# Kernel optimization log

Measured on AMD Instinct MI355X. Metric: run time of the kernel, lower is better.

The kernel has to match this reference:

```python
import jax, jax.numpy as jnp
import numpy as np

EPS = 1e-12

def _layernorm(x, gamma, beta):
    m = jnp.mean(x, axis=-1, keepdims=True)
    v = jnp.mean((x - m) ** 2, axis=-1, keepdims=True)
    return (x - m) * jax.lax.rsqrt(v + EPS) * gamma + beta

def _gcn(x, node_emb, time_emb, W_pool, b_pool, gamma, beta):
    # x: [B, N, C]; node_emb: [N, D]; time_emb: [D]
    e = _layernorm(node_emb + time_emb[None, :], gamma, beta)          # [N, D] (dropout off: eval mode)
    A = jax.nn.softmax(e @ e.T, axis=1)                                 # [N, N] dynamic adjacency
    weights = jnp.einsum('nd,dkio->nkio', e, W_pool)                    # [N, 2, C, O] node-adaptive weights
    bias = e @ b_pool                                                   # [N, O]
    # supports = [I, A]; I support is identity -> x itself
    x_g = jnp.stack([x, jnp.einsum('nm,bmc->bnc', A, x)], axis=2)       # [B, N, 2, C]
    return jnp.einsum('bnki,nkio->bno', x_g, weights) + bias            # [B, N, O]

def setup_inputs() -> dict:
    key = jax.random.key(0)
    ks = jax.random.split(key, 16)
    B, N, Din, H, D = 64, 2048, 2, 64, 16
    C = Din + H
    inp = {
        'x': jax.random.normal(ks[0], (B, N, Din), jnp.float32),
        'state': jax.random.normal(ks[1], (B, N, H), jnp.float32),
        'node_embeddings': jax.random.normal(ks[2], (N, D), jnp.float32),
        'time_embeddings': jax.random.normal(ks[3], (D,), jnp.float32),
    }
    for i, g in enumerate(['z', 'r', 'u']):
        inp[f'W_{g}'] = jax.random.normal(ks[4 + 2 * i], (D, 2, C, H), jnp.float32) * 0.02
        inp[f'b_{g}'] = jax.random.normal(ks[5 + 2 * i], (D, H), jnp.float32) * 0.02
        inp[f'gamma_{g}'] = jnp.ones((D,), jnp.float32)
        inp[f'beta_{g}'] = jnp.zeros((D,), jnp.float32)
    return inp

def reference(x, state, node_embeddings, time_embeddings,
              W_z, b_z, gamma_z, beta_z,
              W_r, b_r, gamma_r, beta_r,
              W_u, b_u, gamma_u, beta_u):
    xs = jnp.concatenate([x, state], axis=-1)                           # [B, N, Din+H]
    z = jax.nn.sigmoid(_gcn(xs, node_embeddings, time_embeddings, W_z, b_z, gamma_z, beta_z))
    r = jax.nn.sigmoid(_gcn(xs, node_embeddings, time_embeddings, W_r, b_r, gamma_r, beta_r))
    cand = jnp.concatenate([x, z * state], axis=-1)
    hc = jnp.tanh(_gcn(cand, node_embeddings, time_embeddings, W_u, b_u, gamma_u, beta_u))
    return r * state + (1.0 - r) * hc
```

## Files before the change

kernel.cpp:

```cpp
#include <hip/hip_runtime.h>
#include <hip/hip_bf16.h>
#include <math.h>


typedef __attribute__((ext_vector_type(4))) float f4;
typedef __attribute__((ext_vector_type(8))) short s8;

#define B_   64
#define N_   2048
#define DIN  2
#define H_   64
#define D_   16
#define C_   66
#define KI   132
#define KIP  160
#define CB   4224

#define GLD16(gp, lp) __builtin_amdgcn_global_load_lds((const __attribute__((address_space(1))) void*)(gp), (__attribute__((address_space(3))) void*)(lp), 16, 0, 0)

static __device__ __forceinline__ ushort f2bf(float v) {
  __hip_bfloat16 h = __float2bfloat16(v);
  return *(ushort*)&h;
}
static __device__ __forceinline__ float bf2f(ushort u) {
  __hip_bfloat16 h = *(__hip_bfloat16*)&u;
  return __bfloat162float(h);
}
static __device__ __forceinline__ uint packbf(float a, float b) {
  return ((uint)f2bf(b) << 16) | f2bf(a);
}

__global__ void k_e(const float* __restrict__ node, const float* __restrict__ timee,
                    const float* __restrict__ g0, const float* __restrict__ b0,
                    const float* __restrict__ g1, const float* __restrict__ b1,
                    const float* __restrict__ g2, const float* __restrict__ b2,
                    float* __restrict__ e, ushort* __restrict__ ebf) {
  int n = blockIdx.x * blockDim.x + threadIdx.x;
  if (n >= N_) return;
  float v[D_]; float m = 0.f;
  #pragma unroll
  for (int d = 0; d < D_; ++d) { v[d] = node[n * D_ + d] + timee[d]; m += v[d]; }
  m *= (1.0f / D_);
  float var = 0.f;
  #pragma unroll
  for (int d = 0; d < D_; ++d) { float t = v[d] - m; var += t * t; }
  var *= (1.0f / D_);
  float r = rsqrtf(var + 1e-12f);
  float y[D_];
  #pragma unroll
  for (int d = 0; d < D_; ++d) y[d] = (v[d] - m) * r;
  const float* gs[3] = {g0, g1, g2};
  const float* bs[3] = {b0, b1, b2};
  #pragma unroll
  for (int g = 0; g < 3; ++g) {
    #pragma unroll
    for (int d = 0; d < D_; d += 2) {
      float o0 = y[d] * gs[g][d] + bs[g][d];
      float o1 = y[d + 1] * gs[g][d + 1] + bs[g][d + 1];
      e[g * N_ * D_ + n * D_ + d] = o0;
      e[g * N_ * D_ + n * D_ + d + 1] = o1;
      *(uint*)&ebf[g * N_ * D_ + n * D_ + d] = packbf(o0, o1);
    }
  }
}

__global__ __launch_bounds__(256)
void k_attn(const ushort* __restrict__ ebf, __hip_bfloat16* __restrict__ A) {
  __shared__ __align__(16) ushort eb[N_ * D_];
  __shared__ float red[4][16];
  const int t = threadIdx.x;
  const ushort* eg = ebf + (size_t)blockIdx.z * (N_ * D_);
  {
    const uint4* src = (const uint4*)eg;
    uint4* dst = (uint4*)eb;
    #pragma unroll
    for (int i = 0; i < 16; ++i) dst[i * 256 + t] = src[i * 256 + t];
  }
  __syncthreads();
  const int lane = t & 63, w = t >> 6;
  const int l15 = lane & 15, q = lane >> 4;
  const int r0 = blockIdx.x * 16;
  s8 rf = {0, 0, 0, 0, 0, 0, 0, 0};
  if (q < 2) rf = *(const s8*)&eb[(r0 + l15) * D_ + q * 8];
  const int c0 = w * 512;
  f4 acc[32];
  #pragma unroll
  for (int tl = 0; tl < 32; ++tl) {
    s8 cf = {0, 0, 0, 0, 0, 0, 0, 0};
    if (q < 2) cf = *(const s8*)&eb[(c0 + tl * 16 + l15) * D_ + q * 8];
    acc[tl] = __builtin_amdgcn_mfma_f32_16x16x32_bf16(cf, rf, (f4)0.0f, 0, 0, 0);
  }
  float m = acc[0][0];
  #pragma unroll
  for (int tl = 0; tl < 32; ++tl) {
    #pragma unroll
    for (int rg = 0; rg < 4; ++rg) m = fmaxf(m, acc[tl][rg]);
  }
  m = fmaxf(m, __shfl_xor(m, 16, 64));
  m = fmaxf(m, __shfl_xor(m, 32, 64));
  if (lane < 16) red[w][l15] = m;
  __syncthreads();
  const float gm = fmaxf(fmaxf(red[0][l15], red[1][l15]), fmaxf(red[2][l15], red[3][l15]));
  __syncthreads();
  float ps = 0.f;
  #pragma unroll
  for (int tl = 0; tl < 32; ++tl) {
    #pragma unroll
    for (int rg = 0; rg < 4; ++rg) {
      float v = __expf(acc[tl][rg] - gm);
      acc[tl][rg] = v;
      ps += v;
    }
  }
  ps += __shfl_xor(ps, 16, 64);
  ps += __shfl_xor(ps, 32, 64);
  if (lane < 16) red[w][l15] = ps;
  __syncthreads();
  const float inv = 1.0f / (red[0][l15] + red[1][l15] + red[2][l15] + red[3][l15]);
  ushort* Ar = (ushort*)A + (size_t)blockIdx.z * ((size_t)N_ * N_) +
               (size_t)(r0 + l15) * N_ + c0 + q * 4;
  #pragma unroll
  for (int tl = 0; tl < 32; ++tl) {
    uint2 pk;
    pk.x = packbf(acc[tl][0] * inv, acc[tl][1] * inv);
    pk.y = packbf(acc[tl][2] * inv, acc[tl][3] * inv);
    *(uint2*)&Ar[tl * 16] = pk;
  }
}

template <int MODE>
__global__ __launch_bounds__(256)
void k_buildX(const float* __restrict__ x, const float* __restrict__ state,
              const __hip_bfloat16* __restrict__ zbuf, __hip_bfloat16* __restrict__ XT) {
  constexpr int LDM = 72;
  __shared__ __align__(16) ushort T[C_ * LDM];
  const int t = threadIdx.x;
  const int m0 = blockIdx.x * 64, b = blockIdx.y;
  const int m = t >> 2, hq = t & 3;
  {
    const float* sp = state + ((size_t)b * N_ + m0 + m) * H_ + hq * 16;
    float sv[16];
    #pragma unroll
    for (int i = 0; i < 16; i += 4) {
      float4 v = *(const float4*)(sp + i);
      sv[i] = v.x; sv[i + 1] = v.y; sv[i + 2] = v.z; sv[i + 3] = v.w;
    }
    if (MODE) {
      const ushort* zp = (const ushort*)zbuf + ((size_t)b * N_ + m0 + m) * H_ + hq * 16;
      uint4 z0 = *(const uint4*)&zp[0], z1 = *(const uint4*)&zp[8];
      uint zw[8] = {z0.x, z0.y, z0.z, z0.w, z1.x, z1.y, z1.z, z1.w};
      #pragma unroll
      for (int i = 0; i < 8; ++i) {
        sv[2 * i]     *= bf2f((ushort)(zw[i] & 0xffffu));
        sv[2 * i + 1] *= bf2f((ushort)(zw[i] >> 16));
      }
    }
    #pragma unroll
    for (int i = 0; i < 16; ++i) T[(DIN + hq * 16 + i) * LDM + m] = f2bf(sv[i]);
    if (t < 64) {
      const float2 xv = *(const float2*)&x[((size_t)b * N_ + m0 + t) * DIN];
      T[0 * LDM + t] = f2bf(xv.x);
      T[1 * LDM + t] = f2bf(xv.y);
    }
  }
  __syncthreads();
  {
    int r = t >> 2, ch = t & 3;
    ushort* dst = (ushort*)XT + (size_t)(b * C_ + r) * N_ + m0 + ch * 16;
    *(uint4*)&dst[0] = *(uint4*)&T[r * LDM + ch * 16];
    *(uint4*)&dst[8] = *(uint4*)&T[r * LDM + ch * 16 + 8];
    if (t < 8) {
      r = 64 + (t >> 2);
      ushort* dst2 = (ushort*)XT + (size_t)(b * C_ + r) * N_ + m0 + ch * 16;
      *(uint4*)&dst2[0] = *(uint4*)&T[r * LDM + ch * 16];
      *(uint4*)&dst2[8] = *(uint4*)&T[r * LDM + ch * 16 + 8];
    }
  }
}

__global__ __launch_bounds__(256)
void k_gemm(const __hip_bfloat16* __restrict__ Abase, size_t astride,
            const __hip_bfloat16* __restrict__ XT,
            __hip_bfloat16* __restrict__ Ybase, size_t ystride) {
  __shared__ __align__(16) ushort At[2][128 * 32];
  __shared__ __align__(16) ushort Xt[2][128 * 32];
  const int t = threadIdx.x;
  const int nwg = gridDim.x * gridDim.y * gridDim.z;
  const int orig = blockIdx.x + gridDim.x * (blockIdx.y + gridDim.y * blockIdx.z);
  const int chunk = nwg >> 3;
  const int swz = (orig & 7) * chunk + (orig >> 3);
  const int bx = swz % gridDim.x;
  const int rest = swz / gridDim.x;
  const int by = rest % gridDim.y;
  const int bz = rest / gridDim.y;
  const int j0 = bx * 128, r0 = by * 128;
  const ushort* Ag = (const ushort*)Abase + (size_t)bz * astride;
  ushort* Y = (ushort*)Ybase + (size_t)bz * ystride;
  const int lane = t & 63, w = t >> 6;
  const int rowa = w * 32 + (lane >> 2);
  const int kc = (((lane & 3) ^ ((lane >> 3) & 3)) * 8);
  const ushort* pA0 = Ag + (size_t)(r0 + rowa) * N_ + kc;
  const ushort* pA1 = pA0 + 16 * N_;
  const ushort* pX0 = (const ushort*)XT + (size_t)(j0 + rowa) * N_ + kc;
  const ushort* pX1 = pX0 + 16 * N_;
  const int l15 = t & 15, q = (t >> 4) & 3;
  const int qs = (q ^ ((l15 >> 1) & 3)) * 8;
  const int wr = (w >> 1) * 64, wc = (w & 1) * 64;
  f4 acc[4][4];
  #pragma unroll
  for (int i = 0; i < 4; ++i)
    #pragma unroll
    for (int jj = 0; jj < 4; ++jj) acc[i][jj] = (f4)0.0f;
  GLD16(pA0, &At[0][(w * 32) * 32]);
  GLD16(pA1, &At[0][(w * 32 + 16) * 32]);
  GLD16(pX0, &Xt[0][(w * 32) * 32]);
  GLD16(pX1, &Xt[0][(w * 32 + 16) * 32]);
  pA0 += 32; pA1 += 32; pX0 += 32; pX1 += 32;
  int cur = 0;
  for (int k0 = 0; k0 < N_; k0 += 32) {
    if (k0 + 32 < N_) {
      const int nx = cur ^ 1;
      GLD16(pA0, &At[nx][(w * 32) * 32]);
      GLD16(pA1, &At[nx][(w * 32 + 16) * 32]);
      GLD16(pX0, &Xt[nx][(w * 32) * 32]);
      GLD16(pX1, &Xt[nx][(w * 32 + 16) * 32]);
      pA0 += 32; pA1 += 32; pX0 += 32; pX1 += 32;
      asm volatile("s_waitcnt vmcnt(4)" ::: "memory");
    } else {
      asm volatile("s_waitcnt vmcnt(0)" ::: "memory");
    }
    __builtin_amdgcn_s_barrier();
    __builtin_amdgcn_sched_barrier(0);
    s8 af[4], bfr[4];
    #pragma unroll
    for (int mi = 0; mi < 4; ++mi)
      af[mi] = *(const s8*)&At[cur][(wr + mi * 16 + l15) * 32 + qs];
    #pragma unroll
    for (int ni = 0; ni < 4; ++ni)
      bfr[ni] = *(const s8*)&Xt[cur][(wc + ni * 16 + l15) * 32 + qs];
    __builtin_amdgcn_s_setprio(1);
    #pragma unroll
    for (int mi = 0; mi < 4; ++mi)
      #pragma unroll
      for (int ni = 0; ni < 4; ++ni)
        acc[mi][ni] = __builtin_amdgcn_mfma_f32_16x16x32_bf16(af[mi], bfr[ni], acc[mi][ni], 0, 0, 0);
    __builtin_amdgcn_s_setprio(0);
    __builtin_amdgcn_s_barrier();
    cur ^= 1;
  }
  #pragma unroll
  for (int mi = 0; mi < 4; ++mi) {
    int rr = r0 + wr + mi * 16 + q * 4;
    #pragma unroll
    for (int ni = 0; ni < 4; ++ni) {
      int cc = j0 + wc + ni * 16 + l15;
      #pragma unroll
      for (int rg = 0; rg < 4; ++rg)
        Y[(size_t)(rr + rg) * CB + cc] = f2bf(acc[mi][ni][rg]);
    }
  }
}

__global__ __launch_bounds__(256)
void k_wmat(const float* __restrict__ eg, const float* __restrict__ Wp, ushort* __restrict__ Wm) {
  constexpr int TRS = 36;
  __shared__ float Wl[16 * 8 * 64];
  __shared__ ushort Tr[8 * 64 * TRS];
  const int t = threadIdx.x;
  const int n0 = blockIdx.x * 8;
  const int y = blockIdx.y;
  const int o = t & 63, w = t >> 6;
  const int ng = w & 1, krh = (w >> 1) * 4;
  float er[4][16];
  #pragma unroll
  for (int j = 0; j < 4; ++j) {
    const float* ep = eg + (size_t)(n0 + ng * 4 + j) * D_;
    #pragma unroll
    for (int d = 0; d < D_; d += 4) {
      float4 v = *(const float4*)(ep + d);
      er[j][d] = v.x; er[j][d + 1] = v.y; er[j][d + 2] = v.z; er[j][d + 3] = v.w;
    }
  }
  const int ngroups = (y == 3) ? 2 : 1;
  for (int g = 0; g < ngroups; ++g) {
    const int kic0 = y * 4 + g * 4;
    for (int kk = 0; kk < 4; ++kk) {
      const int kic = kic0 + kk;
      __syncthreads();
      #pragma unroll
      for (int it = 0; it < 8; ++it) {
        int f = it * 256 + t;
        int d = f >> 7, rem = f & 127, kr = rem >> 4, o4 = rem & 15;
        int ki = kic * 8 + kr;
        float4 v;
        if (ki < KI) v = *(const float4*)&Wp[((size_t)d * KI + ki) * 64 + o4 * 4];
        else { v.x = 0.f; v.y = 0.f; v.z = 0.f; v.w = 0.f; }
        *(float4*)&Wl[f * 4] = v;
      }
      __syncthreads();
      float a[4][4];
      #pragma unroll
      for (int j = 0; j < 4; ++j)
        #pragma unroll
        for (int k = 0; k < 4; ++k) a[j][k] = 0.f;
      for (int d = 0; d < D_; ++d) {
        float w4[4];
        #pragma unroll
        for (int k = 0; k < 4; ++k) w4[k] = Wl[(d * 8 + krh + k) * 64 + o];
        #pragma unroll
        for (int j = 0; j < 4; ++j)
          #pragma unroll
          for (int k = 0; k < 4; ++k) a[j][k] = fmaf(er[j][d], w4[k], a[j][k]);
      }
      #pragma unroll
      for (int j = 0; j < 4; ++j) {
        ushort* tr = &Tr[((ng * 4 + j) * 64 + o) * TRS + kk * 8 + krh];
        *(uint*)&tr[0] = packbf(a[j][0], a[j][1]);
        *(uint*)&tr[2] = packbf(a[j][2], a[j][3]);
      }
    }
    __syncthreads();
    const int k0 = kic0 * 8;
    #pragma unroll
    for (int p = 0; p < 8; ++p) {
      int u = p * 256 + t;
      int nl = u >> 8, oo = (u >> 2) & 63, qq = u & 3;
      const ushort* tr = &Tr[(nl * 64 + oo) * TRS + qq * 8];
      uint2 lo = *(const uint2*)&tr[0];
      uint2 hi = *(const uint2*)&tr[4];
      uint4 vv; vv.x = lo.x; vv.y = lo.y; vv.z = hi.x; vv.w = hi.y;
      *(uint4*)&Wm[((size_t)(n0 + nl) * 64 + oo) * KIP + k0 + qq * 8] = vv;
    }
  }
}

template <int MODE>
__global__ __launch_bounds__(256)
void k_einsum(const float* __restrict__ e, const ushort* __restrict__ Wm, const float* __restrict__ bp,
              const __hip_bfloat16* __restrict__ Y,
              const float* __restrict__ x, const float* __restrict__ state,
              const __hip_bfloat16* __restrict__ zbuf, const __hip_bfloat16* __restrict__ rbuf,
              void* __restrict__ outp) {
  constexpr int LDK = 168;
  constexpr int LDR = 72;
  __shared__ __align__(16) ushort xg[64 * LDK];
  __shared__ __align__(16) ushort res[64 * LDR];
  __shared__ float el[D_];
  __shared__ float bl[64];
  const int n = blockIdx.x, t = threadIdx.x;
  if (t < D_) el[t] = e[n * D_ + t];
  __syncthreads();
  if (t < 64) {
    float s = 0.f;
    #pragma unroll
    for (int d = 0; d < D_; ++d) s += el[d] * bp[d * 64 + t];
    bl[t] = s;
  }
  {
    const int b = t >> 2, j = t & 3;
    const size_t bn = (size_t)b * N_ + n;
    float sv[16];
    const float* sp = state + bn * 64 + j * 16;
    #pragma unroll
    for (int i = 0; i < 16; i += 4) {
      float4 v = *(const float4*)(sp + i);
      sv[i] = v.x; sv[i + 1] = v.y; sv[i + 2] = v.z; sv[i + 3] = v.w;
    }
    if (MODE) {
      const ushort* zp = (const ushort*)zbuf + bn * 64 + j * 16;
      uint4 z0 = *(const uint4*)&zp[0], z1 = *(const uint4*)&zp[8];
      uint zw[8] = {z0.x, z0.y, z0.z, z0.w, z1.x, z1.y, z1.z, z1.w};
      #pragma unroll
      for (int i = 0; i < 8; ++i) {
        sv[2 * i]     *= bf2f((ushort)(zw[i] & 0xffffu));
        sv[2 * i + 1] *= bf2f((ushort)(zw[i] >> 16));
      }
    }
    ushort* xr = &xg[b * LDK + 2 + j * 16];
    #pragma unroll
    for (int i = 0; i < 16; i += 2) {
      uint pk = packbf(sv[i], sv[i + 1]);
      *(uint*)&xr[i] = pk;
    }
    const ushort* yp = (const ushort*)Y + (size_t)n * CB + b * C_ + j * 16;
    uint* xy = (uint*)&xg[b * LDK + 66 + j * 16];
    #pragma unroll
    for (int i = 0; i < 8; ++i) xy[i] = *(const uint*)&yp[2 * i];
    if (j == 0) *(uint*)&xg[b * LDK + 130] = *(const uint*)&yp[64];
    if (t < 64) {
      const float* xp = x + ((size_t)t * N_ + n) * DIN;
      uint pk = packbf(xp[0], xp[1]);
      *(uint*)&xg[t * LDK] = pk;
    }
    ushort* pg = &xg[b * LDK + 132 + j * 7];
    #pragma unroll
    for (int i = 0; i < 7; ++i) pg[i] = 0;
  }
  __syncthreads();
  const int l15 = t & 15, q = (t >> 4) & 3, w = t >> 6;
  const int wm = (w >> 1) * 32, wn = (w & 1) * 32;
  const ushort* Wn = Wm + (size_t)n * (64 * KIP);
  f4 acc[2][2];
  acc[0][0] = acc[0][1] = acc[1][0] = acc[1][1] = (f4)0.0f;
  #pragma unroll
  for (int kk = 0; kk < KIP; kk += 32) {
    s8 af[2], bfr[2];
    #pragma unroll
    for (int mi = 0; mi < 2; ++mi) af[mi] = *(const s8*)&xg[(wm + mi * 16 + l15) * LDK + kk + q * 8];
    #pragma unroll
    for (int ni = 0; ni < 2; ++ni) bfr[ni] = *(const s8*)(Wn + (size_t)(wn + ni * 16 + l15) * KIP + kk + q * 8);
    #pragma unroll
    for (int mi = 0; mi < 2; ++mi)
      #pragma unroll
      for (int ni = 0; ni < 2; ++ni)
        acc[mi][ni] = __builtin_amdgcn_mfma_f32_16x16x32_bf16(af[mi], bfr[ni], acc[mi][ni], 0, 0, 0);
  }
  {
    float bl0 = bl[wn + l15], bl1 = bl[wn + 16 + l15];
    #pragma unroll
    for (int mi = 0; mi < 2; ++mi)
      #pragma unroll
      for (int ni = 0; ni < 2; ++ni) {
        float bb = ni ? bl1 : bl0;
        #pragma unroll
        for (int rg = 0; rg < 4; ++rg) {
          float v = acc[mi][ni][rg] + bb;
          float a;
          if (MODE == 0) a = 1.0f / (1.0f + __expf(-v));
          else           a = 1.0f - 2.0f / (__expf(2.0f * v) + 1.0f);
          res[(wm + mi * 16 + q * 4 + rg) * LDR + (wn + ni * 16 + l15)] = f2bf(a);
        }
      }
  }
  __syncthreads();
  {
    const int b = t >> 2, j = t & 3;
    const size_t gb = ((size_t)b * N_ + n) * 64 + j * 16;
    const ushort* rr = &res[b * LDR + j * 16];
    if (MODE == 0) {
      uint4 v0 = *(const uint4*)&rr[0];
      uint4 v1 = *(const uint4*)&rr[8];
      *(uint4*)((ushort*)outp + gb) = v0;
      *(uint4*)((ushort*)outp + gb + 8) = v1;
    } else {
      float* ob = (float*)outp;
      const float* stp = state + gb;
      const ushort* rp = (const ushort*)rbuf + gb;
      uint4 r0 = *(const uint4*)&rp[0], r1 = *(const uint4*)&rp[8];
      uint rw[8] = {r0.x, r0.y, r0.z, r0.w, r1.x, r1.y, r1.z, r1.w};
      #pragma unroll
      for (int i = 0; i < 16; i += 4) {
        float4 st = *(const float4*)(stp + i);
        float4 ov;
        float rv0 = bf2f((ushort)(rw[i / 2] & 0xffffu));
        float rv1 = bf2f((ushort)(rw[i / 2] >> 16));
        float rv2 = bf2f((ushort)(rw[i / 2 + 1] & 0xffffu));
        float rv3 = bf2f((ushort)(rw[i / 2 + 1] >> 16));
        ov.x = rv0 * st.x + (1.0f - rv0) * bf2f(rr[i]);
        ov.y = rv1 * st.y + (1.0f - rv1) * bf2f(rr[i + 1]);
        ov.z = rv2 * st.z + (1.0f - rv2) * bf2f(rr[i + 2]);
        ov.w = rv3 * st.w + (1.0f - rv3) * bf2f(rr[i + 3]);
        *(float4*)(ob + gb + i) = ov;
      }
    }
  }
}

extern "C" void kernel_launch(void* const* d_in, const int* in_sizes, int n_in,
                              void* d_out, int out_size, void* d_ws, size_t ws_size,
                              hipStream_t stream) {
  const float* x     = (const float*)d_in[0];
  const float* state = (const float*)d_in[1];
  const float* node  = (const float*)d_in[2];
  const float* timee = (const float*)d_in[3];
  const float* W_z = (const float*)d_in[4];
  const float* b_z = (const float*)d_in[5];
  const float* g_z = (const float*)d_in[6];
  const float* be_z = (const float*)d_in[7];
  const float* W_r = (const float*)d_in[8];
  const float* b_r = (const float*)d_in[9];
  const float* g_r = (const float*)d_in[10];
  const float* be_r = (const float*)d_in[11];
  const float* W_u = (const float*)d_in[12];
  const float* b_u = (const float*)d_in[13];
  const float* g_u = (const float*)d_in[14];
  const float* be_u = (const float*)d_in[15];

  constexpr size_t NN = (size_t)N_ * N_;
  constexpr size_t ND = (size_t)N_ * D_;
  char* ws = (char*)d_ws;
  float*           e  = (float*)(ws);
  __hip_bfloat16*  A  = (__hip_bfloat16*)(ws + 393216);
  __hip_bfloat16*  XT = (__hip_bfloat16*)(ws + 25559040);
  __hip_bfloat16*  Y  = (__hip_bfloat16*)(ws + 42860544);
  __hip_bfloat16*  zb = (__hip_bfloat16*)(ws + 60162048);
  __hip_bfloat16*  rb = (__hip_bfloat16*)(ws + 76939264);
  ushort*          ebf = (ushort*)(ws + 93716480);
  ushort*          Wm = (ushort*)(ws + 93716480);
  __hip_bfloat16*  Yr = (__hip_bfloat16*)(ws + 135659520);
  const size_t YRD = ((size_t)135659520 - 42860544) / 2;
  const bool big = ws_size >= (size_t)152961024;

  float* out = (float*)d_out;

  k_e<<<8, 256, 0, stream>>>(node, timee, g_z, be_z, g_r, be_r, g_u, be_u, e, ebf);
  k_attn<<<dim3(N_ / 16, 1, 3), 256, 0, stream>>>(ebf, A);
  k_buildX<0><<<dim3(32, 64), 256, 0, stream>>>(x, state, nullptr, XT);

  dim3 ggrid1(CB / 128, N_ / 128, 1);
  dim3 ggrid2(CB / 128, N_ / 128, 2);
  dim3 wgrid(N_ / 8, 4);

  if (big) {
    k_wmat<<<wgrid, 256, 0, stream>>>(e + 0 * ND, W_z, Wm);
    k_gemm<<<ggrid2, 256, 0, stream>>>(A, NN, XT, Y, YRD);
    k_einsum<0><<<N_, 256, 0, stream>>>(e + 0 * ND, Wm, b_z, Y, x, state, nullptr, nullptr, (void*)zb);
    k_wmat<<<wgrid, 256, 0, stream>>>(e + 1 * ND, W_r, Wm);
    k_einsum<0><<<N_, 256, 0, stream>>>(e + 1 * ND, Wm, b_r, Yr, x, state, nullptr, nullptr, (void*)rb);
  } else {
    k_wmat<<<wgrid, 256, 0, stream>>>(e + 0 * ND, W_z, Wm);
    k_gemm<<<ggrid1, 256, 0, stream>>>(A, 0, XT, Y, 0);
    k_einsum<0><<<N_, 256, 0, stream>>>(e + 0 * ND, Wm, b_z, Y, x, state, nullptr, nullptr, (void*)zb);
    k_wmat<<<wgrid, 256, 0, stream>>>(e + 1 * ND, W_r, Wm);
    k_gemm<<<ggrid1, 256, 0, stream>>>(A + NN, 0, XT, Y, 0);
    k_einsum<0><<<N_, 256, 0, stream>>>(e + 1 * ND, Wm, b_r, Y, x, state, nullptr, nullptr, (void*)rb);
  }
  k_buildX<1><<<dim3(32, 64), 256, 0, stream>>>(x, state, zb, XT);
  k_wmat<<<wgrid, 256, 0, stream>>>(e + 2 * ND, W_u, Wm);
  k_gemm<<<ggrid1, 256, 0, stream>>>(A + 2 * NN, 0, XT, Y, 0);
  k_einsum<1><<<N_, 256, 0, stream>>>(e + 2 * ND, Wm, b_u, Y, x, state, zb, rb, (void*)out);
}
```

Measured before the change: 486.3 us.

## Triple-buffer GEMM LDS loads and rewrite node weight generation with pre-transposed W

The GEMM kernel moves from double to triple buffering of its LDS tiles, with two stages prefetched ahead and vmcnt waits adjusted, so global-memory latency is better hidden. Separately, weight-matrix generation is rewritten. A new k_wcvt kernel transposes W_pool into a [o*KIP+ki][d] float layout, and a simpler k_wmat2 computes each node's bf16 weights with per-thread dot products and no LDS staging. This adds LDS usage, which may cut occupancy, plus extra small transposition launches that reuse workspace regions.

```diff
diff --git a/kernel.cpp b/kernel.cpp
--- a/kernel.cpp
+++ b/kernel.cpp
@@ -15,6 +15,7 @@
 #define KI   132
 #define KIP  160
 #define CB   4224
+#define JW   10240
 
 #define GLD16(gp, lp) __builtin_amdgcn_global_load_lds((const __attribute__((address_space(1))) void*)(gp), (__attribute__((address_space(3))) void*)(lp), 16, 0, 0)
 
@@ -182,8 +183,8 @@
 void k_gemm(const __hip_bfloat16* __restrict__ Abase, size_t astride,
             const __hip_bfloat16* __restrict__ XT,
             __hip_bfloat16* __restrict__ Ybase, size_t ystride) {
-  __shared__ __align__(16) ushort At[2][128 * 32];
-  __shared__ __align__(16) ushort Xt[2][128 * 32];
+  __shared__ __align__(16) ushort At[3][128 * 32];
+  __shared__ __align__(16) ushort Xt[3][128 * 32];
   const int t = threadIdx.x;
   const int nwg = gridDim.x * gridDim.y * gridDim.z;
   const int orig = blockIdx.x + gridDim.x * (blockIdx.y + gridDim.y * blockIdx.z);
@@ -211,20 +212,24 @@
   for (int i = 0; i < 4; ++i)
     #pragma unroll
     for (int jj = 0; jj < 4; ++jj) acc[i][jj] = (f4)0.0f;
-  GLD16(pA0, &At[0][(w * 32) * 32]);
-  GLD16(pA1, &At[0][(w * 32 + 16) * 32]);
-  GLD16(pX0, &Xt[0][(w * 32) * 32]);
-  GLD16(pX1, &Xt[0][(w * 32 + 16) * 32]);
-  pA0 += 32; pA1 += 32; pX0 += 32; pX1 += 32;
-  int cur = 0;
+  #pragma unroll
+  for (int p = 0; p < 2; ++p) {
+    GLD16(pA0, &At[p][(w * 32) * 32]);
+    GLD16(pA1, &At[p][(w * 32 + 16) * 32]);
+    GLD16(pX0, &Xt[p][(w * 32) * 32]);
+    GLD16(pX1, &Xt[p][(w * 32 + 16) * 32]);
+    pA0 += 32; pA1 += 32; pX0 += 32; pX1 += 32;
+  }
+  int cur = 0, nx = 2;
   for (int k0 = 0; k0 < N_; k0 += 32) {
-    if (k0 + 32 < N_) {
-      const int nx = cur ^ 1;
+    if (k0 + 64 < N_) {
       GLD16(pA0, &At[nx][(w * 32) * 32]);
       GLD16(pA1, &At[nx][(w * 32 + 16) * 32]);
       GLD16(pX0, &Xt[nx][(w * 32) * 32]);
       GLD16(pX1, &Xt[nx][(w * 32 + 16) * 32]);
       pA0 += 32; pA1 += 32; pX0 += 32; pX1 += 32;
+      asm volatile("s_waitcnt vmcnt(8)" ::: "memory");
+    } else if (k0 + 32 < N_) {
       asm volatile("s_waitcnt vmcnt(4)" ::: "memory");
     } else {
       asm volatile("s_waitcnt vmcnt(0)" ::: "memory");
@@ -246,7 +251,8 @@
         acc[mi][ni] = __builtin_amdgcn_mfma_f32_16x16x32_bf16(af[mi], bfr[ni], acc[mi][ni], 0, 0, 0);
     __builtin_amdgcn_s_setprio(0);
     __builtin_amdgcn_s_barrier();
-    cur ^= 1;
+    cur = cur == 2 ? 0 : cur + 1;
+    nx = nx == 2 ? 0 : nx + 1;
   }
   #pragma unroll
   for (int mi = 0; mi < 4; ++mi) {
@@ -261,76 +267,49 @@
   }
 }
 
+__global__ void k_wcvt(const float* __restrict__ Wp, float* __restrict__ Wpb) {
+  int j = blockIdx.x * 256 + threadIdx.x;
+  if (j >= JW) return;
+  int o = j / KIP, ki = j - o * KIP;
+  float out[16];
+  #pragma unroll
+  for (int i = 0; i < 16; ++i) out[i] = 0.f;
+  if (ki < KI) {
+    #pragma unroll
+    for (int d = 0; d < 16; ++d) out[d] = Wp[((size_t)d * KI + ki) * 64 + o];
+  }
+  #pragma unroll
+  for (int i = 0; i < 4; ++i) *(float4*)&Wpb[(size_t)j * 16 + i * 4] = *(float4*)&out[i * 4];
+}
+
 __global__ __launch_bounds__(256)
-void k_wmat(const float* __restrict__ eg, const float* __restrict__ Wp, ushort* __restrict__ Wm) {
-  constexpr int TRS = 36;
-  __shared__ float Wl[16 * 8 * 64];
-  __shared__ ushort Tr[8 * 64 * TRS];
+void k_wmat2(const float* __restrict__ eg, const float* __restrict__ Wpb, ushort* __restrict__ Wm) {
   const int t = threadIdx.x;
-  const int n0 = blockIdx.x * 8;
-  const int y = blockIdx.y;
-  const int o = t & 63, w = t >> 6;
-  const int ng = w & 1, krh = (w >> 1) * 4;
-  float er[4][16];
-  #pragma unroll
-  for (int j = 0; j < 4; ++j) {
-    const float* ep = eg + (size_t)(n0 + ng * 4 + j) * D_;
-    #pragma unroll
-    for (int d = 0; d < D_; d += 4) {
-      float4 v = *(const float4*)(ep + d);
-      er[j][d] = v.x; er[j][d + 1] = v.y; er[j][d + 2] = v.z; er[j][d + 3] = v.w;
-    }
-  }
-  const int ngroups = (y == 3) ? 2 : 1;
-  for (int g = 0; g < ngroups; ++g) {
-    const int kic0 = y * 4 + g * 4;
-    for (int kk = 0; kk < 4; ++kk) {
-      const int kic = kic0 + kk;
-      __syncthreads();
-      #pragma unroll
-      for (int it = 0; it < 8; ++it) {
-        int f = it * 256 + t;
-        int d = f >> 7, rem = f & 127, kr = rem >> 4, o4 = rem & 15;
-        int ki = kic * 8 + kr;
-        float4 v;
-        if (ki < KI) v = *(const float4*)&Wp[((size_t)d * KI + ki) * 64 + o4 * 4];
-        else { v.x = 0.f; v.y = 0.f; v.z = 0.f; v.w = 0.f; }
-        *(float4*)&Wl[f * 4] = v;
+  const int n = blockIdx.x * 16 + (t & 15);
+  const int j0 = blockIdx.y * 640 + (t >> 4) * 40;
+  float er[16];
+  const float* ep = eg + (size_t)n * D_;
+  #pragma unroll
+  for (int d = 0; d < 16; d += 4) {
+    float4 v = *(const float4*)(ep + d);
+    er[d] = v.x; er[d + 1] = v.y; er[d + 2] = v.z; er[d + 3] = v.w;
+  }
+  ushort* wrow = Wm + (size_t)n * JW + j0;
+  #pragma unroll
+  for (int c = 0; c < 5; ++c) {
+    ushort ob[8];
+    #pragma unroll
+    for (int u = 0; u < 8; ++u) {
+      const float* wp = Wpb + (size_t)(j0 + c * 8 + u) * 16;
+      float s = 0.f;
+      #pragma unroll
+      for (int d = 0; d < 16; d += 4) {
+        float4 wv = *(const float4*)(wp + d);
+        s = fmaf(er[d], wv.x, fmaf(er[d + 1], wv.y, fmaf(er[d + 2], wv.z, fmaf(er[d + 3], wv.w, s))));
       }
-      __syncthreads();
-      float a[4][4];
-      #pragma unroll
-      for (int j = 0; j < 4; ++j)
-        #pragma unroll
-        for (int k = 0; k < 4; ++k) a[j][k] = 0.f;
-      for (int d = 0; d < D_; ++d) {
-        float w4[4];
-        #pragma unroll
-        for (int k = 0; k < 4; ++k) w4[k] = Wl[(d * 8 + krh + k) * 64 + o];
-        #pragma unroll
-        for (int j = 0; j < 4; ++j)
-          #pragma unroll
-          for (int k = 0; k < 4; ++k) a[j][k] = fmaf(er[j][d], w4[k], a[j][k]);
-      }
-      #pragma unroll
-      for (int j = 0; j < 4; ++j) {
-        ushort* tr = &Tr[((ng * 4 + j) * 64 + o) * TRS + kk * 8 + krh];
-        *(uint*)&tr[0] = packbf(a[j][0], a[j][1]);
-        *(uint*)&tr[2] = packbf(a[j][2], a[j][3]);
-      }
-    }
-    __syncthreads();
-    const int k0 = kic0 * 8;
-    #pragma unroll
-    for (int p = 0; p < 8; ++p) {
-      int u = p * 256 + t;
-      int nl = u >> 8, oo = (u >> 2) & 63, qq = u & 3;
-      const ushort* tr = &Tr[(nl * 64 + oo) * TRS + qq * 8];
-      uint2 lo = *(const uint2*)&tr[0];
-      uint2 hi = *(const uint2*)&tr[4];
-      uint4 vv; vv.x = lo.x; vv.y = lo.y; vv.z = hi.x; vv.w = hi.y;
-      *(uint4*)&Wm[((size_t)(n0 + nl) * 64 + oo) * KIP + k0 + qq * 8] = vv;
-    }
+      ob[u] = f2bf(s);
+    }
+    *(uint4*)&wrow[c * 8] = *(uint4*)&ob[0];
   }
 }
 
@@ -500,33 +479,39 @@
   __hip_bfloat16*  Yr = (__hip_bfloat16*)(ws + 135659520);
   const size_t YRD = ((size_t)135659520 - 42860544) / 2;
   const bool big = ws_size >= (size_t)152961024;
+  float* Wpb_z = (float*)(ws + 60162048);
+  float* Wpb_r = (float*)(ws + 76939264);
+  float* Wpb_u = (float*)(ws + 393216);
 
   float* out = (float*)d_out;
 
   k_e<<<8, 256, 0, stream>>>(node, timee, g_z, be_z, g_r, be_r, g_u, be_u, e, ebf);
   k_attn<<<dim3(N_ / 16, 1, 3), 256, 0, stream>>>(ebf, A);
   k_buildX<0><<<dim3(32, 64), 256, 0, stream>>>(x, state, nullptr, XT);
+  k_wcvt<<<40, 256, 0, stream>>>(W_z, Wpb_z);
+  k_wcvt<<<40, 256, 0, stream>>>(W_r, Wpb_r);
 
   dim3 ggrid1(CB / 128, N_ / 128, 1);
   dim3 ggrid2(CB / 128, N_ / 128, 2);
-  dim3 wgrid(N_ / 8, 4);
+  dim3 wgrid2(N_ / 16, 16);
 
   if (big) {
-    k_wmat<<<wgrid, 256, 0, stream>>>(e + 0 * ND, W_z, Wm);
+    k_wmat2<<<wgrid2, 256, 0, stream>>>(e + 0 * ND, Wpb_z, Wm);
     k_gemm<<<ggrid2, 256, 0, stream>>>(A, NN, XT, Y, YRD);
     k_einsum<0><<<N_, 256, 0, stream>>>(e + 0 * ND, Wm, b_z, Y, x, state, nullptr, nullptr, (void*)zb);
-    k_wmat<<<wgrid, 256, 0, stream>>>(e + 1 * ND, W_r, Wm);
+    k_wmat2<<<wgrid2, 256, 0, stream>>>(e + 1 * ND, Wpb_r, Wm);
     k_einsum<0><<<N_, 256, 0, stream>>>(e + 1 * ND, Wm, b_r, Yr, x, state, nullptr, nullptr, (void*)rb);
   } else {
-    k_wmat<<<wgrid, 256, 0, stream>>>(e + 0 * ND, W_z, Wm);
+    k_wmat2<<<wgrid2, 256, 0, stream>>>(e + 0 * ND, Wpb_z, Wm);
     k_gemm<<<ggrid1, 256, 0, stream>>>(A, 0, XT, Y, 0);
     k_einsum<0><<<N_, 256, 0, stream>>>(e + 0 * ND, Wm, b_z, Y, x, state, nullptr, nullptr, (void*)zb);
-    k_wmat<<<wgrid, 256, 0, stream>>>(e + 1 * ND, W_r, Wm);
+    k_wmat2<<<wgrid2, 256, 0, stream>>>(e + 1 * ND, Wpb_r, Wm);
     k_gemm<<<ggrid1, 256, 0, stream>>>(A + NN, 0, XT, Y, 0);
     k_einsum<0><<<N_, 256, 0, stream>>>(e + 1 * ND, Wm, b_r, Y, x, state, nullptr, nullptr, (void*)rb);
   }
   k_buildX<1><<<dim3(32, 64), 256, 0, stream>>>(x, state, zb, XT);
-  k_wmat<<<wgrid, 256, 0, stream>>>(e + 2 * ND, W_u, Wm);
+  k_wcvt<<<40, 256, 0, stream>>>(W_u, Wpb_u);
+  k_wmat2<<<wgrid2, 256, 0, stream>>>(e + 2 * ND, Wpb_u, Wm);
   k_gemm<<<ggrid1, 256, 0, stream>>>(A + 2 * NN, 0, XT, Y, 0);
   k_einsum<1><<<N_, 256, 0, stream>>>(e + 2 * ND, Wm, b_u, Y, x, state, zb, rb, (void*)out);
 }
```

Result: slower. 533.5 us (+9.7%).
